# Kernel tuning notes

Measured on AMD Instinct MI355X. Metric: run time of the kernel, lower is better.

The kernel has to match this reference:

```python
import jax, jax.numpy as jnp
import numpy as np

TEMPERATURE = 8.0  # sqrt(head_dim=64)

def setup_inputs() -> dict:
    key = jax.random.key(0)
    kq, kk, kv, km = jax.random.split(key, 4)
    B, H, S, D = 2, 16, 2048, 64
    return {
        "query": jax.random.normal(kq, (B, H, S, D), dtype=jnp.float32),
        "key": jax.random.normal(kk, (B, H, S, D), dtype=jnp.float32),
        "value": jax.random.normal(kv, (B, H, S, D), dtype=jnp.float32),
        "mask": jax.random.randint(km, (B, S, S), 0, 2, dtype=jnp.int32),
    }

def reference(query, key, value, mask):
    # energy: [B, H, Sq, Skv]
    energy = jnp.einsum("bhqd,bhkd->bhqk", query, key) / TEMPERATURE
    # mask broadcast over heads; positions where mask == 0 get -10000
    energy = jnp.where(mask[:, None, :, :] == 0, jnp.float32(-10000.0), energy)
    attention = jax.nn.softmax(energy, axis=-1)
    # replicate the module's NaN cleanup (softmax over all -inf rows)
    attention = jnp.where(jnp.isnan(attention), jnp.float32(0.0), attention)
    # dropout is identity in eval/deterministic mode
    out = jnp.einsum("bhqk,bhkd->bhqd", attention, value)
    return out, attention
```

## Files before the change

kernel.cpp:

```cpp
#include <hip/hip_runtime.h>

typedef __attribute__((ext_vector_type(8))) short short8;
typedef __attribute__((ext_vector_type(4))) short bf16x4;
typedef __attribute__((ext_vector_type(4))) float floatx4;

#define MFMA_QK(a, b, c) __builtin_amdgcn_mfma_f32_16x16x32_bf16((a), (b), (c), 0, 0, 0)
#define MFMA_PV(a, b, c) __builtin_amdgcn_mfma_f32_16x16x16bf16_1k((a), (b), (c), 0, 0, 0)

static constexpr int Bn = 2, Hn = 16, Sn = 2048, Dn = 64;
static constexpr int QT = 64;
static constexpr int KT = 32;
static constexpr int NIT = Sn / KT;
static constexpr int KS_LD = 72;
static constexpr int VT_LD = 40;

__device__ __forceinline__ ushort f2bf(float f) {
    union { float f; unsigned int u; } c; c.f = f;
    unsigned int u = c.u;
    u += 0x7FFFu + ((u >> 16) & 1u);
    return (ushort)(u >> 16);
}

__device__ __forceinline__ short8 pack8(float4 a, float4 b) {
    short8 r;
    r[0] = (short)f2bf(a.x); r[1] = (short)f2bf(a.y);
    r[2] = (short)f2bf(a.z); r[3] = (short)f2bf(a.w);
    r[4] = (short)f2bf(b.x); r[5] = (short)f2bf(b.y);
    r[6] = (short)f2bf(b.z); r[7] = (short)f2bf(b.w);
    return r;
}

__device__ __forceinline__ void wg_barrier() {
    asm volatile("s_waitcnt lgkmcnt(0)" ::: "memory");
    __builtin_amdgcn_s_barrier();
    asm volatile("" ::: "memory");
}

__global__ __launch_bounds__(256, 4) void sdpa_kernel(
    const float* __restrict__ Q,
    const float* __restrict__ K,
    const float* __restrict__ V,
    const int*   __restrict__ M,
    float* __restrict__ O,
    float* __restrict__ A)
{
    const int qt = blockIdx.x, h = blockIdx.y, b = blockIdx.z;
    const int tid  = threadIdx.x;
    const int wave = tid >> 6;
    const int lane = tid & 63;
    const int l16  = lane & 15;
    const int quad = lane >> 4;
    const int l16h = l16 >> 3;

    const size_t head = (size_t)(b * Hn + h) * Sn * Dn;
    const float* Qh = Q + head;
    const float* Kh = K + head;
    const float* Vh = V + head;
    const int qg0 = qt * QT + wave * 16;
    const int* Mb = M + (size_t)b * Sn * Sn;
    float* Ahead = A + (size_t)(b * Hn + h) * Sn * Sn;
    float* Ohead = O + head;

    __shared__ short KsA[2][KT * KS_LD];
    __shared__ short VTb[2][Dn * VT_LD];

    short8 qf[2];
    {
        const float* qp = Qh + (size_t)(qg0 + l16) * Dn;
        qf[0] = pack8(*(const float4*)(qp + quad * 8), *(const float4*)(qp + quad * 8 + 4));
        qf[1] = pack8(*(const float4*)(qp + 32 + quad * 8), *(const float4*)(qp + 36 + quad * 8));
    }

    const int srow = tid >> 3;
    const int scol = (tid & 7) * 8;
    const int vidx = (((tid >> 6) ^ (tid & 3)) << 3) + (srow & 7);

    const int* Mrow0 = Mb + (size_t)(qg0 + l16) * Sn;
    float* Arow0 = Ahead + (size_t)(qg0 + l16) * Sn;

    float psum = 0.f;
    floatx4 z0 = {0.f, 0.f, 0.f, 0.f};
    floatx4 oacc[4] = {z0, z0, z0, z0};
    {
        const float* kst = Kh + (size_t)srow * Dn + scol;
        const float* vst = Vh + (size_t)srow * Dn + scol;
        {
            float4 a = *(const float4*)kst;  float4 c = *(const float4*)(kst + 4);
            *(short8*)&KsA[0][srow * KS_LD + scol] = pack8(a, c);
            float4 d = *(const float4*)vst;  float4 e = *(const float4*)(vst + 4);
            short* vp = &VTb[0][scol * VT_LD + vidx];
            vp[0 * VT_LD] = (short)f2bf(d.x); vp[1 * VT_LD] = (short)f2bf(d.y);
            vp[2 * VT_LD] = (short)f2bf(d.z); vp[3 * VT_LD] = (short)f2bf(d.w);
            vp[4 * VT_LD] = (short)f2bf(e.x); vp[5 * VT_LD] = (short)f2bf(e.y);
            vp[6 * VT_LD] = (short)f2bf(e.z); vp[7 * VT_LD] = (short)f2bf(e.w);
        }
        kst += KT * Dn; vst += KT * Dn;
        float4 ka = *(const float4*)kst, kb = *(const float4*)(kst + 4);
        float4 va = *(const float4*)vst, vb = *(const float4*)(vst + 4);
        kst += KT * Dn; vst += KT * Dn;
        __syncthreads();

        short* kc = KsA[0]; short* kn = KsA[1];
        short* vc = VTb[0]; short* vn = VTb[1];

        for (int it = 0; it < NIT; ++it) {
            if (it + 1 < NIT) {
                *(short8*)&kn[srow * KS_LD + scol] = pack8(ka, kb);
                short* vp = &vn[scol * VT_LD + vidx];
                vp[0 * VT_LD] = (short)f2bf(va.x); vp[1 * VT_LD] = (short)f2bf(va.y);
                vp[2 * VT_LD] = (short)f2bf(va.z); vp[3 * VT_LD] = (short)f2bf(va.w);
                vp[4 * VT_LD] = (short)f2bf(vb.x); vp[5 * VT_LD] = (short)f2bf(vb.y);
                vp[6 * VT_LD] = (short)f2bf(vb.z); vp[7 * VT_LD] = (short)f2bf(vb.w);
            }
            if (it + 2 < NIT) {
                ka = *(const float4*)kst; kb = *(const float4*)(kst + 4);
                va = *(const float4*)vst; vb = *(const float4*)(vst + 4);
                kst += KT * Dn; vst += KT * Dn;
            }

            floatx4 z = {0.f, 0.f, 0.f, 0.f};
            floatx4 sc[2] = {z, z};
            #pragma unroll
            for (int t = 0; t < 2; ++t)
                #pragma unroll
                for (int c = 0; c < 2; ++c) {
                    short8 kf = *(const short8*)&kc[(t * 16 + l16) * KS_LD + c * 32 + quad * 8];
                    sc[t] = MFMA_QK(kf, qf[c], sc[t]);
                }

            const int* mrp = Mrow0 + it * KT + (quad << 2);
            const int4 m0 = *(const int4*)mrp;
            const int4 m1 = *(const int4*)(mrp + 16);

            float pt0[4], pt1[4];
            pt0[0] = __expf(m0.x ? sc[0][0] * 0.125f : -10000.0f);
            pt0[1] = __expf(m0.y ? sc[0][1] * 0.125f : -10000.0f);
            pt0[2] = __expf(m0.z ? sc[0][2] * 0.125f : -10000.0f);
            pt0[3] = __expf(m0.w ? sc[0][3] * 0.125f : -10000.0f);
            pt1[0] = __expf(m1.x ? sc[1][0] * 0.125f : -10000.0f);
            pt1[1] = __expf(m1.y ? sc[1][1] * 0.125f : -10000.0f);
            pt1[2] = __expf(m1.z ? sc[1][2] * 0.125f : -10000.0f);
            pt1[3] = __expf(m1.w ? sc[1][3] * 0.125f : -10000.0f);
            psum += (pt0[0] + pt0[1]) + (pt0[2] + pt0[3])
                  + (pt1[0] + pt1[1]) + (pt1[2] + pt1[3]);

            bf16x4 af0 = { (short)f2bf(pt0[0]), (short)f2bf(pt0[1]),
                           (short)f2bf(pt0[2]), (short)f2bf(pt0[3]) };
            bf16x4 af1 = { (short)f2bf(pt1[0]), (short)f2bf(pt1[1]),
                           (short)f2bf(pt1[2]), (short)f2bf(pt1[3]) };

            #pragma unroll
            for (int tn = 0; tn < 4; ++tn) {
                const int row = tn * 16 + l16;
                const int dg  = (2 * tn + l16h) & 3;
                const int base = row * VT_LD + ((quad & 1) << 2);
                bf16x4 vf0 = *(const bf16x4*)&vc[base + ((((quad >> 1)) ^ dg) << 3)];
                oacc[tn] = MFMA_PV(af0, vf0, oacc[tn]);
                bf16x4 vf1 = *(const bf16x4*)&vc[base + (((2 + (quad >> 1)) ^ dg) << 3)];
                oacc[tn] = MFMA_PV(af1, vf1, oacc[tn]);
            }

            wg_barrier();
            short* t1 = kc; kc = kn; kn = t1;
            short* t2 = vc; vc = vn; vn = t2;
        }
    }

    float s = psum;
    s += __shfl_xor(s, 16);
    s += __shfl_xor(s, 32);
    const float invl = s > 0.f ? 1.0f / s : 0.f;

    float invo[4];
    #pragma unroll
    for (int r = 0; r < 4; ++r) invo[r] = __shfl(invl, (quad << 2) + r);
    #pragma unroll
    for (int tn = 0; tn < 4; ++tn)
        #pragma unroll
        for (int r = 0; r < 4; ++r)
            Ohead[(size_t)(qg0 + (quad << 2) + r) * Dn + tn * 16 + l16] =
                oacc[tn][r] * invo[r];

    {
        const float* kst = Kh + (size_t)srow * Dn + scol;
        {
            float4 a = *(const float4*)kst;  float4 c = *(const float4*)(kst + 4);
            *(short8*)&KsA[0][srow * KS_LD + scol] = pack8(a, c);
        }
        kst += KT * Dn;
        float4 ka = *(const float4*)kst, kb = *(const float4*)(kst + 4);
        kst += KT * Dn;
        __syncthreads();

        short* kc = KsA[0]; short* kn = KsA[1];

        for (int it = 0; it < NIT; ++it) {
            if (it + 1 < NIT)
                *(short8*)&kn[srow * KS_LD + scol] = pack8(ka, kb);
            if (it + 2 < NIT) {
                ka = *(const float4*)kst; kb = *(const float4*)(kst + 4);
                kst += KT * Dn;
            }

            floatx4 z = {0.f, 0.f, 0.f, 0.f};
            floatx4 sc[2] = {z, z};
            #pragma unroll
            for (int t = 0; t < 2; ++t)
                #pragma unroll
                for (int c = 0; c < 2; ++c) {
                    short8 kf = *(const short8*)&kc[(t * 16 + l16) * KS_LD + c * 32 + quad * 8];
                    sc[t] = MFMA_QK(kf, qf[c], sc[t]);
                }

            const int* mrp = Mrow0 + it * KT + (quad << 2);
            const int4 m0 = *(const int4*)mrp;
            const int4 m1 = *(const int4*)(mrp + 16);

            float4 p0, p1;
            p0.x = __expf(m0.x ? sc[0][0] * 0.125f : -10000.0f) * invl;
            p0.y = __expf(m0.y ? sc[0][1] * 0.125f : -10000.0f) * invl;
            p0.z = __expf(m0.z ? sc[0][2] * 0.125f : -10000.0f) * invl;
            p0.w = __expf(m0.w ? sc[0][3] * 0.125f : -10000.0f) * invl;
            p1.x = __expf(m1.x ? sc[1][0] * 0.125f : -10000.0f) * invl;
            p1.y = __expf(m1.y ? sc[1][1] * 0.125f : -10000.0f) * invl;
            p1.z = __expf(m1.z ? sc[1][2] * 0.125f : -10000.0f) * invl;
            p1.w = __expf(m1.w ? sc[1][3] * 0.125f : -10000.0f) * invl;

            *(float4*)&Arow0[it * KT + (quad << 2)]      = p0;
            *(float4*)&Arow0[it * KT + 16 + (quad << 2)] = p1;

            wg_barrier();
            short* t1 = kc; kc = kn; kn = t1;
        }
    }
}

extern "C" void kernel_launch(void* const* d_in, const int* in_sizes, int n_in,
                              void* d_out, int out_size, void* d_ws, size_t ws_size,
                              hipStream_t stream) {
    const float* Q = (const float*)d_in[0];
    const float* K = (const float*)d_in[1];
    const float* V = (const float*)d_in[2];
    const int*   M = (const int*)d_in[3];
    float* O = (float*)d_out;
    float* A = O + (size_t)Bn * Hn * Sn * Dn;
    dim3 grid(Sn / QT, Hn, Bn);
    sdpa_kernel<<<grid, 256, 0, stream>>>(Q, K, V, M, O, A);
}
```

Measured before the change: 802.3 us.

## Precompute bf16 K and transposed V in prep kernel; prefetch masks, stream attention stores

A new prep kernel converts K to bf16 and writes V transposed in bf16 to workspace, so the main kernel loads half the bytes and no longer converts or transposes in its inner loop. The second pass reads K fragments straight from global into registers with a double buffer, dropping LDS staging and barriers. It also adds mask prefetch one iteration ahead, s_setprio around the MFMA blocks, packed bf16 conversion via v_cvt_pk_bf16_f32, and nontemporal stores for the attention matrix. This adds an extra launch and workspace traffic, and the second pass relies on cache hits for the repeated K reads.

```diff
diff --git a/kernel.cpp b/kernel.cpp
--- a/kernel.cpp
+++ b/kernel.cpp
@@ -30,19 +30,66 @@
     return r;
 }
 
+__device__ __forceinline__ bf16x4 cvt4(float a, float b, float c, float d) {
+    unsigned int lo, hi;
+    asm("v_cvt_pk_bf16_f32 %0, %1, %2" : "=v"(lo) : "v"(a), "v"(b));
+    asm("v_cvt_pk_bf16_f32 %0, %1, %2" : "=v"(hi) : "v"(c), "v"(d));
+    union { unsigned int u[2]; bf16x4 v; } r;
+    r.u[0] = lo; r.u[1] = hi;
+    return r.v;
+}
+
 __device__ __forceinline__ void wg_barrier() {
     asm volatile("s_waitcnt lgkmcnt(0)" ::: "memory");
     __builtin_amdgcn_s_barrier();
     asm volatile("" ::: "memory");
 }
 
+__global__ __launch_bounds__(256) void prep_kernel(
+    const float* __restrict__ K, const float* __restrict__ V,
+    ushort* __restrict__ Kbf, ushort* __restrict__ Vt)
+{
+    const int kc = blockIdx.x, h = blockIdx.y, b = blockIdx.z;
+    const size_t head = (size_t)(b * Hn + h) * Sn * Dn;
+    const int k0 = kc * 64;
+    const int tid = threadIdx.x;
+    const int r  = tid >> 2;
+    const int c0 = (tid & 3) << 4;
+
+    __shared__ ushort T[64][72];
+
+    const float* kp = K + head + (size_t)(k0 + r) * Dn + c0;
+    const float* vp = V + head + (size_t)(k0 + r) * Dn + c0;
+
+    short8 ks0 = pack8(*(const float4*)kp, *(const float4*)(kp + 4));
+    short8 ks1 = pack8(*(const float4*)(kp + 8), *(const float4*)(kp + 12));
+    ushort* ko = Kbf + head + (size_t)(k0 + r) * Dn + c0;
+    *(short8*)(ko)     = ks0;
+    *(short8*)(ko + 8) = ks1;
+
+    short8 vs0 = pack8(*(const float4*)vp, *(const float4*)(vp + 4));
+    short8 vs1 = pack8(*(const float4*)(vp + 8), *(const float4*)(vp + 12));
+    *(short8*)&T[r][c0]     = vs0;
+    *(short8*)&T[r][c0 + 8] = vs1;
+    __syncthreads();
+
+    const int d  = tid >> 2;
+    const int kk = (tid & 3) << 4;
+    union { ushort u[16]; short8 s[2]; } o;
+    #pragma unroll
+    for (int j = 0; j < 16; ++j) o.u[j] = T[kk + j][d];
+    ushort* vo = Vt + head + (size_t)d * Sn + k0 + kk;
+    *(short8*)(vo)     = o.s[0];
+    *(short8*)(vo + 8) = o.s[1];
+}
+
 __global__ __launch_bounds__(256, 4) void sdpa_kernel(
     const float* __restrict__ Q,
-    const float* __restrict__ K,
-    const float* __restrict__ V,
     const int*   __restrict__ M,
     float* __restrict__ O,
-    float* __restrict__ A)
+    float* __restrict__ A,
+    const ushort* __restrict__ Kbf,
+    const ushort* __restrict__ Vt)
 {
     const int qt = blockIdx.x, h = blockIdx.y, b = blockIdx.z;
     const int tid  = threadIdx.x;
@@ -54,8 +101,8 @@
 
     const size_t head = (size_t)(b * Hn + h) * Sn * Dn;
     const float* Qh = Q + head;
-    const float* Kh = K + head;
-    const float* Vh = V + head;
+    const ushort* Kbfh = Kbf + head;
+    const ushort* Vth  = Vt + head;
     const int qg0 = qt * QT + wave * 16;
     const int* Mb = M + (size_t)b * Sn * Sn;
     float* Ahead = A + (size_t)(b * Hn + h) * Sn * Sn;
@@ -73,7 +120,9 @@
 
     const int srow = tid >> 3;
     const int scol = (tid & 7) * 8;
-    const int vidx = (((tid >> 6) ^ (tid & 3)) << 3) + (srow & 7);
+    const int vrow = tid >> 2;
+    const int vcol = (tid & 3) << 3;
+    const int vblk = (((tid & 3) ^ ((vrow >> 3) & 3)) << 3);
 
     const int* Mrow0 = Mb + (size_t)(qg0 + l16) * Sn;
     float* Arow0 = Ahead + (size_t)(qg0 + l16) * Sn;
@@ -82,44 +131,46 @@
     floatx4 z0 = {0.f, 0.f, 0.f, 0.f};
     floatx4 oacc[4] = {z0, z0, z0, z0};
     {
-        const float* kst = Kh + (size_t)srow * Dn + scol;
-        const float* vst = Vh + (size_t)srow * Dn + scol;
+        const ushort* kp = Kbfh + (size_t)srow * Dn + scol;
+        const ushort* vp = Vth + (size_t)vrow * Sn + vcol;
         {
-            float4 a = *(const float4*)kst;  float4 c = *(const float4*)(kst + 4);
-            *(short8*)&KsA[0][srow * KS_LD + scol] = pack8(a, c);
-            float4 d = *(const float4*)vst;  float4 e = *(const float4*)(vst + 4);
-            short* vp = &VTb[0][scol * VT_LD + vidx];
-            vp[0 * VT_LD] = (short)f2bf(d.x); vp[1 * VT_LD] = (short)f2bf(d.y);
-            vp[2 * VT_LD] = (short)f2bf(d.z); vp[3 * VT_LD] = (short)f2bf(d.w);
-            vp[4 * VT_LD] = (short)f2bf(e.x); vp[5 * VT_LD] = (short)f2bf(e.y);
-            vp[6 * VT_LD] = (short)f2bf(e.z); vp[7 * VT_LD] = (short)f2bf(e.w);
+            short8 k0r = *(const short8*)kp;
+            short8 v0r = *(const short8*)vp;
+            *(short8*)&KsA[0][srow * KS_LD + scol] = k0r;
+            *(short8*)&VTb[0][vrow * VT_LD + vblk] = v0r;
         }
-        kst += KT * Dn; vst += KT * Dn;
-        float4 ka = *(const float4*)kst, kb = *(const float4*)(kst + 4);
-        float4 va = *(const float4*)vst, vb = *(const float4*)(vst + 4);
-        kst += KT * Dn; vst += KT * Dn;
+        kp += KT * Dn; vp += KT;
+        short8 kreg = *(const short8*)kp;
+        short8 vreg = *(const short8*)vp;
+        kp += KT * Dn; vp += KT;
+
+        int4 m0 = *(const int4*)(Mrow0 + (quad << 2));
+        int4 m1 = *(const int4*)(Mrow0 + 16 + (quad << 2));
+
         __syncthreads();
-
         short* kc = KsA[0]; short* kn = KsA[1];
         short* vc = VTb[0]; short* vn = VTb[1];
 
         for (int it = 0; it < NIT; ++it) {
             if (it + 1 < NIT) {
-                *(short8*)&kn[srow * KS_LD + scol] = pack8(ka, kb);
-                short* vp = &vn[scol * VT_LD + vidx];
-                vp[0 * VT_LD] = (short)f2bf(va.x); vp[1 * VT_LD] = (short)f2bf(va.y);
-                vp[2 * VT_LD] = (short)f2bf(va.z); vp[3 * VT_LD] = (short)f2bf(va.w);
-                vp[4 * VT_LD] = (short)f2bf(vb.x); vp[5 * VT_LD] = (short)f2bf(vb.y);
-                vp[6 * VT_LD] = (short)f2bf(vb.z); vp[7 * VT_LD] = (short)f2bf(vb.w);
+                *(short8*)&kn[srow * KS_LD + scol] = kreg;
+                *(short8*)&vn[vrow * VT_LD + vblk] = vreg;
             }
             if (it + 2 < NIT) {
-                ka = *(const float4*)kst; kb = *(const float4*)(kst + 4);
-                va = *(const float4*)vst; vb = *(const float4*)(vst + 4);
-                kst += KT * Dn; vst += KT * Dn;
-            }
-
-            floatx4 z = {0.f, 0.f, 0.f, 0.f};
-            floatx4 sc[2] = {z, z};
+                kreg = *(const short8*)kp;
+                vreg = *(const short8*)vp;
+                kp += KT * Dn; vp += KT;
+            }
+            int4 m0n = m0, m1n = m1;
+            if (it + 1 < NIT) {
+                const int* mrp = Mrow0 + (it + 1) * KT + (quad << 2);
+                m0n = *(const int4*)mrp;
+                m1n = *(const int4*)(mrp + 16);
+            }
+
+            floatx4 zz = {0.f, 0.f, 0.f, 0.f};
+            floatx4 sc[2] = {zz, zz};
+            __builtin_amdgcn_s_setprio(1);
             #pragma unroll
             for (int t = 0; t < 2; ++t)
                 #pragma unroll
@@ -127,10 +178,7 @@
                     short8 kf = *(const short8*)&kc[(t * 16 + l16) * KS_LD + c * 32 + quad * 8];
                     sc[t] = MFMA_QK(kf, qf[c], sc[t]);
                 }
-
-            const int* mrp = Mrow0 + it * KT + (quad << 2);
-            const int4 m0 = *(const int4*)mrp;
-            const int4 m1 = *(const int4*)(mrp + 16);
+            __builtin_amdgcn_s_setprio(0);
 
             float pt0[4], pt1[4];
             pt0[0] = __expf(m0.x ? sc[0][0] * 0.125f : -10000.0f);
@@ -144,11 +192,10 @@
             psum += (pt0[0] + pt0[1]) + (pt0[2] + pt0[3])
                   + (pt1[0] + pt1[1]) + (pt1[2] + pt1[3]);
 
-            bf16x4 af0 = { (short)f2bf(pt0[0]), (short)f2bf(pt0[1]),
-                           (short)f2bf(pt0[2]), (short)f2bf(pt0[3]) };
-            bf16x4 af1 = { (short)f2bf(pt1[0]), (short)f2bf(pt1[1]),
-                           (short)f2bf(pt1[2]), (short)f2bf(pt1[3]) };
-
+            bf16x4 af0 = cvt4(pt0[0], pt0[1], pt0[2], pt0[3]);
+            bf16x4 af1 = cvt4(pt1[0], pt1[1], pt1[2], pt1[3]);
+
+            __builtin_amdgcn_s_setprio(1);
             #pragma unroll
             for (int tn = 0; tn < 4; ++tn) {
                 const int row = tn * 16 + l16;
@@ -159,7 +206,9 @@
                 bf16x4 vf1 = *(const bf16x4*)&vc[base + (((2 + (quad >> 1)) ^ dg) << 3)];
                 oacc[tn] = MFMA_PV(af1, vf1, oacc[tn]);
             }
-
+            __builtin_amdgcn_s_setprio(0);
+
+            m0 = m0n; m1 = m1n;
             wg_barrier();
             short* t1 = kc; kc = kn; kn = t1;
             short* t2 = vc; vc = vn; vn = t2;
@@ -182,55 +231,60 @@
                 oacc[tn][r] * invo[r];
 
     {
-        const float* kst = Kh + (size_t)srow * Dn + scol;
-        {
-            float4 a = *(const float4*)kst;  float4 c = *(const float4*)(kst + 4);
-            *(short8*)&KsA[0][srow * KS_LD + scol] = pack8(a, c);
-        }
-        kst += KT * Dn;
-        float4 ka = *(const float4*)kst, kb = *(const float4*)(kst + 4);
-        kst += KT * Dn;
-        __syncthreads();
-
-        short* kc = KsA[0]; short* kn = KsA[1];
+        const ushort* kb = Kbfh + (size_t)l16 * Dn + (quad << 3);
+        short8 cur[2][2], nxt[2][2];
+        #pragma unroll
+        for (int t = 0; t < 2; ++t)
+            #pragma unroll
+            for (int c = 0; c < 2; ++c)
+                cur[t][c] = *(const short8*)(kb + (size_t)(t * 16) * Dn + c * 32);
+
+        int4 m0 = *(const int4*)(Mrow0 + (quad << 2));
+        int4 m1 = *(const int4*)(Mrow0 + 16 + (quad << 2));
 
         for (int it = 0; it < NIT; ++it) {
-            if (it + 1 < NIT)
-                *(short8*)&kn[srow * KS_LD + scol] = pack8(ka, kb);
-            if (it + 2 < NIT) {
-                ka = *(const float4*)kst; kb = *(const float4*)(kst + 4);
-                kst += KT * Dn;
-            }
-
-            floatx4 z = {0.f, 0.f, 0.f, 0.f};
-            floatx4 sc[2] = {z, z};
+            int4 m0n = m0, m1n = m1;
+            if (it + 1 < NIT) {
+                const ushort* kb1 = kb + (size_t)((it + 1) * KT) * Dn;
+                #pragma unroll
+                for (int t = 0; t < 2; ++t)
+                    #pragma unroll
+                    for (int c = 0; c < 2; ++c)
+                        nxt[t][c] = *(const short8*)(kb1 + (size_t)(t * 16) * Dn + c * 32);
+                const int* mrp = Mrow0 + (it + 1) * KT + (quad << 2);
+                m0n = *(const int4*)mrp;
+                m1n = *(const int4*)(mrp + 16);
+            }
+
+            floatx4 zz = {0.f, 0.f, 0.f, 0.f};
+            floatx4 sc[2] = {zz, zz};
+            __builtin_amdgcn_s_setprio(1);
             #pragma unroll
             for (int t = 0; t < 2; ++t)
                 #pragma unroll
-                for (int c = 0; c < 2; ++c) {
-                    short8 kf = *(const short8*)&kc[(t * 16 + l16) * KS_LD + c * 32 + quad * 8];
-                    sc[t] = MFMA_QK(kf, qf[c], sc[t]);
-                }
-
-            const int* mrp = Mrow0 + it * KT + (quad << 2);
-            const int4 m0 = *(const int4*)mrp;
-            const int4 m1 = *(const int4*)(mrp + 16);
-
-            float4 p0, p1;
-            p0.x = __expf(m0.x ? sc[0][0] * 0.125f : -10000.0f) * invl;
-            p0.y = __expf(m0.y ? sc[0][1] * 0.125f : -10000.0f) * invl;
-            p0.z = __expf(m0.z ? sc[0][2] * 0.125f : -10000.0f) * invl;
-            p0.w = __expf(m0.w ? sc[0][3] * 0.125f : -10000.0f) * invl;
-            p1.x = __expf(m1.x ? sc[1][0] * 0.125f : -10000.0f) * invl;
-            p1.y = __expf(m1.y ? sc[1][1] * 0.125f : -10000.0f) * invl;
-            p1.z = __expf(m1.z ? sc[1][2] * 0.125f : -10000.0f) * invl;
-            p1.w = __expf(m1.w ? sc[1][3] * 0.125f : -10000.0f) * invl;
-
-            *(float4*)&Arow0[it * KT + (quad << 2)]      = p0;
-            *(float4*)&Arow0[it * KT + 16 + (quad << 2)] = p1;
-
-            wg_barrier();
-            short* t1 = kc; kc = kn; kn = t1;
+                for (int c = 0; c < 2; ++c)
+                    sc[t] = MFMA_QK(cur[t][c], qf[c], sc[t]);
+            __builtin_amdgcn_s_setprio(0);
+
+            floatx4 p0, p1;
+            p0[0] = __expf(m0.x ? sc[0][0] * 0.125f : -10000.0f) * invl;
+            p0[1] = __expf(m0.y ? sc[0][1] * 0.125f : -10000.0f) * invl;
+            p0[2] = __expf(m0.z ? sc[0][2] * 0.125f : -10000.0f) * invl;
+            p0[3] = __expf(m0.w ? sc[0][3] * 0.125f : -10000.0f) * invl;
+            p1[0] = __expf(m1.x ? sc[1][0] * 0.125f : -10000.0f) * invl;
+            p1[1] = __expf(m1.y ? sc[1][1] * 0.125f : -10000.0f) * invl;
+            p1[2] = __expf(m1.z ? sc[1][2] * 0.125f : -10000.0f) * invl;
+            p1[3] = __expf(m1.w ? sc[1][3] * 0.125f : -10000.0f) * invl;
+
+            __builtin_nontemporal_store(p0, (floatx4*)&Arow0[it * KT + (quad << 2)]);
+            __builtin_nontemporal_store(p1, (floatx4*)&Arow0[it * KT + 16 + (quad << 2)]);
+
+            #pragma unroll
+            for (int t = 0; t < 2; ++t)
+                #pragma unroll
+                for (int c = 0; c < 2; ++c)
+                    cur[t][c] = nxt[t][c];
+            m0 = m0n; m1 = m1n;
         }
     }
 }
@@ -244,6 +298,13 @@
     const int*   M = (const int*)d_in[3];
     float* O = (float*)d_out;
     float* A = O + (size_t)Bn * Hn * Sn * Dn;
+
+    ushort* Kbf = (ushort*)d_ws;
+    ushort* Vt  = Kbf + (size_t)Bn * Hn * Sn * Dn;
+
+    dim3 pgrid(Sn / 64, Hn, Bn);
+    prep_kernel<<<pgrid, 256, 0, stream>>>(K, V, Kbf, Vt);
+
     dim3 grid(Sn / QT, Hn, Bn);
-    sdpa_kernel<<<grid, 256, 0, stream>>>(Q, K, V, M, O, A);
-}
+    sdpa_kernel<<<grid, 256, 0, stream>>>(Q, M, O, A, Kbf, Vt);
+}
```

Measured after the change: 780.9 us. 1.03x faster.
